# Kernel tuning notes

Measured on AMD Instinct MI355X. Metric: run time of the kernel, lower is better.

Reference implementation:

```python
import jax, jax.numpy as jnp
import numpy as np

EMSIZE = 1024
NHEAD = 16
HEAD = EMSIZE // NHEAD


def setup_inputs() -> dict:
    key = jax.random.key(0)
    ks = jax.random.split(key, 8)
    s = 1.0 / np.sqrt(EMSIZE)
    return {
        "embed": jax.random.normal(ks[0], (2, 2048, EMSIZE), dtype=jnp.float32),
        "q": jax.random.normal(ks[1], (2, 2048, EMSIZE), dtype=jnp.float32),
        "Wk": jax.random.normal(ks[2], (EMSIZE, EMSIZE), dtype=jnp.float32) * s,
        "bk": jnp.zeros((EMSIZE,), dtype=jnp.float32),
        "Wq": jax.random.normal(ks[3], (EMSIZE, EMSIZE), dtype=jnp.float32) * s,
        "bq": jnp.zeros((EMSIZE,), dtype=jnp.float32),
        "Wv": jax.random.normal(ks[4], (EMSIZE, EMSIZE), dtype=jnp.float32) * s,
        "bv": jnp.zeros((EMSIZE,), dtype=jnp.float32),
    }


def _split_heads(x):
    # [b, s, E] -> [b, h, s, d]
    b, s, _ = x.shape
    return x.reshape(b, s, NHEAD, HEAD).transpose(0, 2, 1, 3)


def reference(embed, q, Wk, bk, Wq, bq, Wv, bv):
    # torch Linear: y = x @ W.T + b
    k = _split_heads(embed @ Wk.T + bk)   # [b, h, skv, d]
    qh = _split_heads(q @ Wq.T + bq)      # [b, h, sq, d]
    v = _split_heads(embed @ Wv.T + bv)   # [b, h, skv, d]
    scale = 1.0 / np.sqrt(HEAD).astype(np.float32)
    scores = jnp.einsum("bhqd,bhkd->bhqk", qh, k) * scale
    attn = jax.nn.softmax(scores, axis=-1)  # dropout p=0 -> identity
    ctx = jnp.einsum("bhqk,bhkd->bhqd", attn, v)
    b, h, sq, d = ctx.shape
    return ctx.transpose(0, 2, 1, 3).reshape(b, sq, h * d)
```

## Files before the change

### kernel.cpp

```cpp
#include <hip/hip_runtime.h>
#include <cstdint>
#include <cstddef>


using bf16 = __bf16;
typedef __bf16 bf16x8 __attribute__((ext_vector_type(8)));
typedef float f32x4 __attribute__((ext_vector_type(4)));
typedef short short4v __attribute__((ext_vector_type(4)));

__device__ __forceinline__ void async16(void* lds, const void* g) {
  __builtin_amdgcn_global_load_lds((__attribute__((address_space(1))) void*)g,
                                   (__attribute__((address_space(3))) void*)lds,
                                   16, 0, 0);
}

__device__ __forceinline__ short bf16_bits(float f) {
  bf16 h = (bf16)f;
  union { bf16 h; short s; } u; u.h = h;
  return u.s;
}

__global__ void cast_all_kernel(const float* __restrict__ e, const float* __restrict__ q,
                                const float* __restrict__ wk, const float* __restrict__ wq,
                                const float* __restrict__ wv, bf16* __restrict__ dst) {
  int i = blockIdx.x * blockDim.x + threadIdx.x;
  if (i >= 2883584) return;
  const float* src; int off;
  if (i < 1048576)      { src = e;  off = 0; }
  else if (i < 2097152) { src = q;  off = 1048576; }
  else if (i < 2359296) { src = wk; off = 2097152; }
  else if (i < 2621440) { src = wq; off = 2359296; }
  else                  { src = wv; off = 2621440; }
  float4 v = reinterpret_cast<const float4*>(src)[i - off];
  union { bf16 h[4]; unsigned long long u; } o;
  o.h[0] = (bf16)v.x; o.h[1] = (bf16)v.y; o.h[2] = (bf16)v.z; o.h[3] = (bf16)v.w;
  reinterpret_cast<unsigned long long*>(dst)[i] = o.u;
}

__global__ __launch_bounds__(256) void proj_kernel(
    const bf16* __restrict__ emb, const bf16* __restrict__ qin,
    const bf16* __restrict__ wk, const bf16* __restrict__ wq, const bf16* __restrict__ wv,
    const float* __restrict__ bk, const float* __restrict__ bq, const float* __restrict__ bv,
    bf16* __restrict__ Kp, bf16* __restrict__ Qp, bf16* __restrict__ Vt)
{
  __shared__ bf16 As[128 * 64];
  __shared__ bf16 Bs[128 * 64];

  int pid = blockIdx.x;
  int proj = pid >> 8;
  int t = pid & 255;
  int m0 = (t >> 3) * 128;
  int n0 = (t & 7) * 128;

  const bf16* A = (proj == 1) ? qin : emb;
  const bf16* W = (proj == 0) ? wk : (proj == 1) ? wq : wv;
  const float* bias = (proj == 0) ? bk : (proj == 1) ? bq : bv;
  const bool proj2 = (proj == 2);

  int tid = threadIdx.x;
  int lane = tid & 63, wid = tid >> 6;
  int quad = lane >> 4, l16 = lane & 15;
  int moff = (wid & 1) * 64, noff = (wid >> 1) * 64;

  f32x4 zero = {0.f, 0.f, 0.f, 0.f};
  f32x4 acc[4][4];
#pragma unroll
  for (int i = 0; i < 4; i++)
#pragma unroll
    for (int j = 0; j < 4; j++) acc[i][j] = zero;

  for (int kk = 0; kk < 1024; kk += 64) {
    __syncthreads();
#pragma unroll
    for (int i = 0; i < 4; i++) {
      int c = i * 256 + tid;
      int row = c >> 3;
      int ko = ((c ^ row) & 7) << 3;
      async16(&As[(size_t)(i * 256 + wid * 64) * 8], &A[(size_t)(m0 + row) * 1024 + kk + ko]);
      async16(&Bs[(size_t)(i * 256 + wid * 64) * 8], &W[(size_t)(n0 + row) * 1024 + kk + ko]);
    }
    __syncthreads();
#pragma unroll
    for (int ks = 0; ks < 2; ks++) {
      bf16x8 af[4], bfr[4];
#pragma unroll
      for (int i = 0; i < 4; i++) {
        int row = moff + i * 16 + l16;
        af[i] = *reinterpret_cast<const bf16x8*>(&As[row * 64 + ((((ks << 2) | quad) ^ row) & 7) * 8]);
      }
#pragma unroll
      for (int j = 0; j < 4; j++) {
        int row = noff + j * 16 + l16;
        bfr[j] = *reinterpret_cast<const bf16x8*>(&Bs[row * 64 + ((((ks << 2) | quad) ^ row) & 7) * 8]);
      }
      if (proj2) {
#pragma unroll
        for (int i = 0; i < 4; i++)
#pragma unroll
          for (int j = 0; j < 4; j++)
            acc[i][j] = __builtin_amdgcn_mfma_f32_16x16x32_bf16(bfr[j], af[i], acc[i][j], 0, 0, 0);
      } else {
#pragma unroll
        for (int i = 0; i < 4; i++)
#pragma unroll
          for (int j = 0; j < 4; j++)
            acc[i][j] = __builtin_amdgcn_mfma_f32_16x16x32_bf16(af[i], bfr[j], acc[i][j], 0, 0, 0);
      }
    }
  }

  if (proj2) {
#pragma unroll
    for (int i = 0; i < 4; i++) {
      int grow = m0 + moff + i * 16 + l16;
      int bb = grow >> 11;
      int ss = grow & 2047;
#pragma unroll
      for (int j = 0; j < 4; j++) {
#pragma unroll
        for (int r = 0; r < 4; r++) {
          int gcol = n0 + noff + j * 16 + quad * 4 + r;
          int hh = gcol >> 6, dd = gcol & 63;
          int bh = bb * 16 + hh;
          float v = acc[i][j][r] + bias[gcol];
          Vt[((size_t)bh * 64 + dd) * 2048 + ss] = (bf16)v;
        }
      }
    }
  } else {
    float bvv[4];
#pragma unroll
    for (int j = 0; j < 4; j++) bvv[j] = bias[n0 + noff + j * 16 + l16];
    bf16* dst = (proj == 0) ? Kp : Qp;
#pragma unroll
    for (int i = 0; i < 4; i++) {
#pragma unroll
      for (int r = 0; r < 4; r++) {
        int grow = m0 + moff + i * 16 + quad * 4 + r;
        int bb = grow >> 11;
        int ss = grow & 2047;
#pragma unroll
        for (int j = 0; j < 4; j++) {
          int gcol = n0 + noff + j * 16 + l16;
          int hh = gcol >> 6, dd = gcol & 63;
          int bh = bb * 16 + hh;
          float v = acc[i][j][r] + bvv[j];
          dst[((size_t)bh * 2048 + ss) * 64 + dd] = (bf16)v;
        }
      }
    }
  }
}

__global__ __launch_bounds__(256, 2) void attn_kernel(
    const bf16* __restrict__ Qp, const bf16* __restrict__ Kp, const bf16* __restrict__ Vt,
    float* __restrict__ out)
{
  __shared__ bf16 Ks[2][128 * 64];
  __shared__ bf16 Vs[2][64 * 128];

  int bid = blockIdx.x;
  int bh = bid >> 4;
  int q0 = (bid & 15) << 7;
  int bb = bh >> 4, hh = bh & 15;

  const bf16* Qg = Qp + (size_t)bh * (2048 * 64);
  const bf16* Kg = Kp + (size_t)bh * (2048 * 64);
  const bf16* Vg = Vt + (size_t)bh * (64 * 2048);

  int tid = threadIdx.x, lane = tid & 63, wid = tid >> 6;
  int quad = lane >> 4, l16 = lane & 15;
  int wq0 = q0 + wid * 32;

  auto stage = [&](int kt_, int buf) {
#pragma unroll
    for (int i = 0; i < 4; i++) {
      int c = i * 256 + tid;
      int rk = c >> 3;
      int ko = ((c ^ rk) & 7) << 3;
      async16(&Ks[buf][(size_t)(i * 256 + wid * 64) * 8], &Kg[(size_t)(kt_ * 128 + rk) * 64 + ko]);
      int rv = c >> 4;
      int so = (((c & 15) ^ rv) & 15) << 3;
      async16(&Vs[buf][(size_t)(i * 256 + wid * 64) * 8], &Vg[(size_t)rv * 2048 + kt_ * 128 + so]);
    }
  };

  bf16x8 qf[2][2];
#pragma unroll
  for (int qt = 0; qt < 2; qt++)
#pragma unroll
    for (int ks = 0; ks < 2; ks++)
      qf[qt][ks] = *reinterpret_cast<const bf16x8*>(
          &Qg[(size_t)(wq0 + qt * 16 + l16) * 64 + ks * 32 + quad * 8]);

  stage(0, 0);

  f32x4 zero = {0.f, 0.f, 0.f, 0.f};
  f32x4 O[2][4];
#pragma unroll
  for (int qt = 0; qt < 2; qt++)
#pragma unroll
    for (int dt = 0; dt < 4; dt++) O[qt][dt] = zero;
  float m_i[2] = {-1e30f, -1e30f};
  float l_i[2] = {0.f, 0.f};

  for (int kt = 0; kt < 16; kt++) {
    int cur = kt & 1;
    __syncthreads();
    __builtin_amdgcn_sched_barrier(0);
    if (kt < 15) stage(kt + 1, cur ^ 1);
    __builtin_amdgcn_sched_barrier(0);

    const bf16* Kc = Ks[cur];
    const bf16* Vc = Vs[cur];

    f32x4 Sf[2][8];
#pragma unroll
    for (int n = 0; n < 8; n++) {
      int row = n * 16 + l16;
      bf16x8 kf0 = *reinterpret_cast<const bf16x8*>(&Kc[row * 64 + ((quad ^ row) & 7) * 8]);
      bf16x8 kf1 = *reinterpret_cast<const bf16x8*>(&Kc[row * 64 + (((4 | quad) ^ row) & 7) * 8]);
#pragma unroll
      for (int qt = 0; qt < 2; qt++) {
        f32x4 s = zero;
        s = __builtin_amdgcn_mfma_f32_16x16x32_bf16(kf0, qf[qt][0], s, 0, 0, 0);
        s = __builtin_amdgcn_mfma_f32_16x16x32_bf16(kf1, qf[qt][1], s, 0, 0, 0);
        Sf[qt][n] = s;
      }
    }

#pragma unroll
    for (int qt = 0; qt < 2; qt++) {
      float mx = -1e30f;
#pragma unroll
      for (int n = 0; n < 8; n++)
#pragma unroll
        for (int r = 0; r < 4; r++) mx = fmaxf(mx, Sf[qt][n][r]);
      mx = fmaxf(mx, __shfl_xor(mx, 16));
      mx = fmaxf(mx, __shfl_xor(mx, 32));
      float mnew = fmaxf(m_i[qt], mx);
      float a = __expf((m_i[qt] - mnew) * 0.125f);
      m_i[qt] = mnew;
      float rs = 0.f;
#pragma unroll
      for (int n = 0; n < 8; n++)
#pragma unroll
        for (int r = 0; r < 4; r++) {
          float p = __expf((Sf[qt][n][r] - mnew) * 0.125f);
          Sf[qt][n][r] = p;
          rs += p;
        }
      rs += __shfl_xor(rs, 16);
      rs += __shfl_xor(rs, 32);
      l_i[qt] = l_i[qt] * a + rs;
#pragma unroll
      for (int dt = 0; dt < 4; dt++)
#pragma unroll
        for (int r = 0; r < 4; r++) O[qt][dt][r] *= a;
    }

#pragma unroll
    for (int n = 0; n < 8; n++) {
      short4v pf[2];
#pragma unroll
      for (int qt = 0; qt < 2; qt++) {
        union { short s[4]; short4v v; } u;
#pragma unroll
        for (int r = 0; r < 4; r++) u.s[r] = bf16_bits(Sf[qt][n][r]);
        pf[qt] = u.v;
      }
      int cj = n * 2 + (quad >> 1);
      int sub = (quad & 1) * 4;
#pragma unroll
      for (int dt = 0; dt < 4; dt++) {
        int rowv = dt * 16 + l16;
        short4v vf = *reinterpret_cast<const short4v*>(
            &Vc[rowv * 128 + (((cj ^ rowv) & 15) << 3) + sub]);
        O[0][dt] = __builtin_amdgcn_mfma_f32_16x16x16bf16_1k(vf, pf[0], O[0][dt], 0, 0, 0);
        O[1][dt] = __builtin_amdgcn_mfma_f32_16x16x16bf16_1k(vf, pf[1], O[1][dt], 0, 0, 0);
      }
    }
  }

#pragma unroll
  for (int qt = 0; qt < 2; qt++) {
    float inv = 1.0f / l_i[qt];
    int qrow = wq0 + qt * 16 + l16;
    float* dst = out + ((size_t)bb * 2048 + qrow) * 1024 + hh * 64;
#pragma unroll
    for (int dt = 0; dt < 4; dt++) {
      float4 o;
      o.x = O[qt][dt][0] * inv;
      o.y = O[qt][dt][1] * inv;
      o.z = O[qt][dt][2] * inv;
      o.w = O[qt][dt][3] * inv;
      *reinterpret_cast<float4*>(&dst[dt * 16 + quad * 4]) = o;
    }
  }
}

extern "C" void kernel_launch(void* const* d_in, const int* in_sizes, int n_in,
                              void* d_out, int out_size, void* d_ws, size_t ws_size,
                              hipStream_t stream) {
  (void)in_sizes; (void)n_in; (void)out_size; (void)ws_size;
  const float* embed = (const float*)d_in[0];
  const float* qin   = (const float*)d_in[1];
  const float* Wk    = (const float*)d_in[2];
  const float* bk    = (const float*)d_in[3];
  const float* Wq    = (const float*)d_in[4];
  const float* bq    = (const float*)d_in[5];
  const float* Wv    = (const float*)d_in[6];
  const float* bv    = (const float*)d_in[7];
  float* out = (float*)d_out;

  bf16* ws = (bf16*)d_ws;
  bf16* emb_bf = ws;
  bf16* q_bf   = emb_bf + 4194304;
  bf16* wk_bf  = q_bf   + 4194304;
  bf16* wq_bf  = wk_bf  + 1048576;
  bf16* wv_bf  = wq_bf  + 1048576;
  bf16* Kp     = wv_bf  + 1048576;
  bf16* Qp     = Kp     + 4194304;
  bf16* Vt     = Qp     + 4194304;

  cast_all_kernel<<<11264, 256, 0, stream>>>(embed, qin, Wk, Wq, Wv, ws);

  proj_kernel<<<768, 256, 0, stream>>>(emb_bf, q_bf, wk_bf, wq_bf, wv_bf,
                                       bk, bq, bv, Kp, Qp, Vt);
  attn_kernel<<<512, 256, 0, stream>>>(Qp, Kp, Vt, out);
}
```

Measured before the change: 199.8 us.

## Switch attention to 32x32x16 MFMA with 64-key tiles and prescaled Q

Rewrites the attention inner loop to use 32x32x16 bf16 MFMA for both QK^T and PV. P is kept in registers, with a lane-swap shuffle to rearrange it into B-operand layout. The KV tile shrinks from 128 to 64 keys, cutting LDS, and launch bounds rise to 3 blocks per SM. The 1/sqrt(d) scale moves into the Q projection epilogue, removing the per-element multiply in the softmax. The cost is more loop iterations and barriers, plus extra cross-lane shuffles for the P repacking.

```diff
diff --git a/kernel.cpp b/kernel.cpp
--- a/kernel.cpp
+++ b/kernel.cpp
@@ -6,7 +6,8 @@
 using bf16 = __bf16;
 typedef __bf16 bf16x8 __attribute__((ext_vector_type(8)));
 typedef float f32x4 __attribute__((ext_vector_type(4)));
-typedef short short4v __attribute__((ext_vector_type(4)));
+typedef float f32x16 __attribute__((ext_vector_type(16)));
+using uint32 = unsigned int;
 
 __device__ __forceinline__ void async16(void* lds, const void* g) {
   __builtin_amdgcn_global_load_lds((__attribute__((address_space(1))) void*)g,
@@ -14,10 +15,10 @@
                                    16, 0, 0);
 }
 
-__device__ __forceinline__ short bf16_bits(float f) {
-  bf16 h = (bf16)f;
-  union { bf16 h; short s; } u; u.h = h;
-  return u.s;
+__device__ __forceinline__ uint32 pack_bf16x2(float lo, float hi_) {
+  union { bf16 h[2]; uint32 u; } w;
+  w.h[0] = (bf16)lo; w.h[1] = (bf16)hi_;
+  return w.u;
 }
 
 __global__ void cast_all_kernel(const float* __restrict__ e, const float* __restrict__ q,
@@ -132,6 +133,7 @@
 #pragma unroll
     for (int j = 0; j < 4; j++) bvv[j] = bias[n0 + noff + j * 16 + l16];
     bf16* dst = (proj == 0) ? Kp : Qp;
+    const float qs = (proj == 1) ? 0.125f : 1.0f;
 #pragma unroll
     for (int i = 0; i < 4; i++) {
 #pragma unroll
@@ -144,7 +146,7 @@
           int gcol = n0 + noff + j * 16 + l16;
           int hh = gcol >> 6, dd = gcol & 63;
           int bh = bb * 16 + hh;
-          float v = acc[i][j][r] + bvv[j];
+          float v = (acc[i][j][r] + bvv[j]) * qs;
           dst[((size_t)bh * 2048 + ss) * 64 + dd] = (bf16)v;
         }
       }
@@ -152,12 +154,12 @@
   }
 }
 
-__global__ __launch_bounds__(256, 2) void attn_kernel(
+__global__ __launch_bounds__(256, 3) void attn_kernel(
     const bf16* __restrict__ Qp, const bf16* __restrict__ Kp, const bf16* __restrict__ Vt,
     float* __restrict__ out)
 {
-  __shared__ bf16 Ks[2][128 * 64];
-  __shared__ bf16 Vs[2][64 * 128];
+  __shared__ bf16 Ks[2][64 * 64];
+  __shared__ bf16 Vs[2][64 * 64];
 
   int bid = blockIdx.x;
   int bh = bid >> 4;
@@ -169,134 +171,123 @@
   const bf16* Vg = Vt + (size_t)bh * (64 * 2048);
 
   int tid = threadIdx.x, lane = tid & 63, wid = tid >> 6;
-  int quad = lane >> 4, l16 = lane & 15;
+  int l32 = lane & 31;
+  int h = lane >> 5;
+  bool hi_half = (h != 0);
   int wq0 = q0 + wid * 32;
 
   auto stage = [&](int kt_, int buf) {
 #pragma unroll
-    for (int i = 0; i < 4; i++) {
+    for (int i = 0; i < 2; i++) {
       int c = i * 256 + tid;
-      int rk = c >> 3;
-      int ko = ((c ^ rk) & 7) << 3;
-      async16(&Ks[buf][(size_t)(i * 256 + wid * 64) * 8], &Kg[(size_t)(kt_ * 128 + rk) * 64 + ko]);
-      int rv = c >> 4;
-      int so = (((c & 15) ^ rv) & 15) << 3;
-      async16(&Vs[buf][(size_t)(i * 256 + wid * 64) * 8], &Vg[(size_t)rv * 2048 + kt_ * 128 + so]);
+      int row = c >> 3;
+      int ko = ((c ^ row) & 7) << 3;
+      async16(&Ks[buf][(size_t)(i * 256 + wid * 64) * 8], &Kg[(size_t)(kt_ * 64 + row) * 64 + ko]);
+      async16(&Vs[buf][(size_t)(i * 256 + wid * 64) * 8], &Vg[(size_t)row * 2048 + kt_ * 64 + ko]);
     }
   };
 
-  bf16x8 qf[2][2];
-#pragma unroll
-  for (int qt = 0; qt < 2; qt++)
-#pragma unroll
-    for (int ks = 0; ks < 2; ks++)
-      qf[qt][ks] = *reinterpret_cast<const bf16x8*>(
-          &Qg[(size_t)(wq0 + qt * 16 + l16) * 64 + ks * 32 + quad * 8]);
+  bf16x8 qf[4];
+#pragma unroll
+  for (int s = 0; s < 4; s++)
+    qf[s] = *reinterpret_cast<const bf16x8*>(
+        &Qg[(size_t)(wq0 + l32) * 64 + s * 16 + h * 8]);
 
   stage(0, 0);
 
-  f32x4 zero = {0.f, 0.f, 0.f, 0.f};
-  f32x4 O[2][4];
-#pragma unroll
-  for (int qt = 0; qt < 2; qt++)
-#pragma unroll
-    for (int dt = 0; dt < 4; dt++) O[qt][dt] = zero;
-  float m_i[2] = {-1e30f, -1e30f};
-  float l_i[2] = {0.f, 0.f};
-
-  for (int kt = 0; kt < 16; kt++) {
+  f32x16 Ov[2];
+#pragma unroll
+  for (int i = 0; i < 16; i++) { Ov[0][i] = 0.f; Ov[1][i] = 0.f; }
+  float m_i = -1e30f, l_i = 0.f;
+
+  for (int kt = 0; kt < 32; kt++) {
     int cur = kt & 1;
     __syncthreads();
     __builtin_amdgcn_sched_barrier(0);
-    if (kt < 15) stage(kt + 1, cur ^ 1);
+    if (kt < 31) stage(kt + 1, cur ^ 1);
     __builtin_amdgcn_sched_barrier(0);
 
     const bf16* Kc = Ks[cur];
     const bf16* Vc = Vs[cur];
 
-    f32x4 Sf[2][8];
-#pragma unroll
-    for (int n = 0; n < 8; n++) {
-      int row = n * 16 + l16;
-      bf16x8 kf0 = *reinterpret_cast<const bf16x8*>(&Kc[row * 64 + ((quad ^ row) & 7) * 8]);
-      bf16x8 kf1 = *reinterpret_cast<const bf16x8*>(&Kc[row * 64 + (((4 | quad) ^ row) & 7) * 8]);
-#pragma unroll
-      for (int qt = 0; qt < 2; qt++) {
-        f32x4 s = zero;
-        s = __builtin_amdgcn_mfma_f32_16x16x32_bf16(kf0, qf[qt][0], s, 0, 0, 0);
-        s = __builtin_amdgcn_mfma_f32_16x16x32_bf16(kf1, qf[qt][1], s, 0, 0, 0);
-        Sf[qt][n] = s;
-      }
-    }
-
-#pragma unroll
-    for (int qt = 0; qt < 2; qt++) {
-      float mx = -1e30f;
-#pragma unroll
-      for (int n = 0; n < 8; n++)
-#pragma unroll
-        for (int r = 0; r < 4; r++) mx = fmaxf(mx, Sf[qt][n][r]);
-      mx = fmaxf(mx, __shfl_xor(mx, 16));
-      mx = fmaxf(mx, __shfl_xor(mx, 32));
-      float mnew = fmaxf(m_i[qt], mx);
-      float a = __expf((m_i[qt] - mnew) * 0.125f);
-      m_i[qt] = mnew;
-      float rs = 0.f;
-#pragma unroll
-      for (int n = 0; n < 8; n++)
-#pragma unroll
-        for (int r = 0; r < 4; r++) {
-          float p = __expf((Sf[qt][n][r] - mnew) * 0.125f);
-          Sf[qt][n][r] = p;
-          rs += p;
-        }
-      rs += __shfl_xor(rs, 16);
-      rs += __shfl_xor(rs, 32);
-      l_i[qt] = l_i[qt] * a + rs;
-#pragma unroll
-      for (int dt = 0; dt < 4; dt++)
-#pragma unroll
-        for (int r = 0; r < 4; r++) O[qt][dt][r] *= a;
-    }
-
-#pragma unroll
-    for (int n = 0; n < 8; n++) {
-      short4v pf[2];
-#pragma unroll
-      for (int qt = 0; qt < 2; qt++) {
-        union { short s[4]; short4v v; } u;
-#pragma unroll
-        for (int r = 0; r < 4; r++) u.s[r] = bf16_bits(Sf[qt][n][r]);
-        pf[qt] = u.v;
-      }
-      int cj = n * 2 + (quad >> 1);
-      int sub = (quad & 1) * 4;
-#pragma unroll
-      for (int dt = 0; dt < 4; dt++) {
-        int rowv = dt * 16 + l16;
-        short4v vf = *reinterpret_cast<const short4v*>(
-            &Vc[rowv * 128 + (((cj ^ rowv) & 15) << 3) + sub]);
-        O[0][dt] = __builtin_amdgcn_mfma_f32_16x16x16bf16_1k(vf, pf[0], O[0][dt], 0, 0, 0);
-        O[1][dt] = __builtin_amdgcn_mfma_f32_16x16x16bf16_1k(vf, pf[1], O[1][dt], 0, 0, 0);
+    f32x16 St[2];
+#pragma unroll
+    for (int t = 0; t < 2; t++) {
+#pragma unroll
+      for (int i = 0; i < 16; i++) St[t][i] = 0.f;
+#pragma unroll
+      for (int s = 0; s < 4; s++) {
+        int row = t * 32 + l32;
+        int j8 = s * 2 + h;
+        bf16x8 kf = *reinterpret_cast<const bf16x8*>(&Kc[row * 64 + ((j8 ^ row) & 7) * 8]);
+        St[t] = __builtin_amdgcn_mfma_f32_32x32x16_bf16(kf, qf[s], St[t], 0, 0, 0);
+      }
+    }
+
+    float mx = -1e30f;
+#pragma unroll
+    for (int t = 0; t < 2; t++)
+#pragma unroll
+      for (int i = 0; i < 16; i++) mx = fmaxf(mx, St[t][i]);
+    mx = fmaxf(mx, __shfl_xor(mx, 32));
+    float mnew = fmaxf(m_i, mx);
+    float a = __expf(m_i - mnew);
+    m_i = mnew;
+    float rs = 0.f;
+#pragma unroll
+    for (int t = 0; t < 2; t++)
+#pragma unroll
+      for (int i = 0; i < 16; i++) {
+        float p = __expf(St[t][i] - mnew);
+        St[t][i] = p;
+        rs += p;
+      }
+    rs += __shfl_xor(rs, 32);
+    l_i = l_i * a + rs;
+#pragma unroll
+    for (int i = 0; i < 16; i++) { Ov[0][i] *= a; Ov[1][i] *= a; }
+
+    uint32 pk[2][8], spk[2][8];
+#pragma unroll
+    for (int t = 0; t < 2; t++)
+#pragma unroll
+      for (int i = 0; i < 8; i++) {
+        pk[t][i] = pack_bf16x2(St[t][2 * i], St[t][2 * i + 1]);
+        spk[t][i] = (uint32)__shfl_xor((int)pk[t][i], 32);
+      }
+
+#pragma unroll
+    for (int k = 0; k < 4; k++) {
+      int t = k >> 1, sub = k & 1;
+      union { uint32 u[4]; bf16x8 v; } pb;
+      pb.u[0] = hi_half ? spk[t][2 + 4 * sub] : pk[t][0 + 4 * sub];
+      pb.u[1] = hi_half ? spk[t][3 + 4 * sub] : pk[t][1 + 4 * sub];
+      pb.u[2] = hi_half ? pk[t][2 + 4 * sub] : spk[t][0 + 4 * sub];
+      pb.u[3] = hi_half ? pk[t][3 + 4 * sub] : spk[t][1 + 4 * sub];
+#pragma unroll
+      for (int dt = 0; dt < 2; dt++) {
+        int row = dt * 32 + l32;
+        int j8 = k * 2 + h;
+        bf16x8 vf = *reinterpret_cast<const bf16x8*>(&Vc[row * 64 + ((j8 ^ row) & 7) * 8]);
+        Ov[dt] = __builtin_amdgcn_mfma_f32_32x32x16_bf16(vf, pb.v, Ov[dt], 0, 0, 0);
       }
     }
   }
 
-#pragma unroll
-  for (int qt = 0; qt < 2; qt++) {
-    float inv = 1.0f / l_i[qt];
-    int qrow = wq0 + qt * 16 + l16;
-    float* dst = out + ((size_t)bb * 2048 + qrow) * 1024 + hh * 64;
-#pragma unroll
-    for (int dt = 0; dt < 4; dt++) {
+  float inv = 1.0f / l_i;
+  int q = wq0 + l32;
+  float* dst = out + ((size_t)bb * 2048 + q) * 1024 + hh * 64;
+#pragma unroll
+  for (int dt = 0; dt < 2; dt++)
+#pragma unroll
+    for (int g = 0; g < 4; g++) {
       float4 o;
-      o.x = O[qt][dt][0] * inv;
-      o.y = O[qt][dt][1] * inv;
-      o.z = O[qt][dt][2] * inv;
-      o.w = O[qt][dt][3] * inv;
-      *reinterpret_cast<float4*>(&dst[dt * 16 + quad * 4]) = o;
-    }
-  }
+      o.x = Ov[dt][4 * g + 0] * inv;
+      o.y = Ov[dt][4 * g + 1] * inv;
+      o.z = Ov[dt][4 * g + 2] * inv;
+      o.w = Ov[dt][4 * g + 3] * inv;
+      *reinterpret_cast<float4*>(&dst[dt * 32 + g * 8 + 4 * h]) = o;
+    }
 }
 
 extern "C" void kernel_launch(void* const* d_in, const int* in_sizes, int n_in,
```

Result: slower. 205.9 us (+3.1%).
